# Kernel optimization log

Measured on AMD Instinct MI355X. Metric: run time of the kernel, lower is better.

The kernel has to match this reference:

```python
import jax, jax.numpy as jnp
import numpy as np

B, M, N, D = 2, 2048, 2048, 2048
N_H, D_H, D_R = 16, 128, 64
THETA = 1000000.0
SCALE = 1.0 / np.sqrt(D_H + D_R)


def build_rope_cache(seq_len, dim, theta):
    freqs = 1.0 / theta ** (jnp.arange(0, dim, 2, dtype=jnp.float32) / dim)
    t = jnp.arange(seq_len, dtype=jnp.float32)
    freqs = jnp.outer(t, freqs)  # (S, dim//2)
    cos = jnp.repeat(jnp.cos(freqs), 2, axis=-1)  # (S, dim)
    sin = jnp.repeat(jnp.sin(freqs), 2, axis=-1)
    return cos, sin


def apply_rope(x, cos, sin):
    # x: (..., S, dim); cos/sin broadcastable (S, dim)
    x_rot = jnp.stack([-x[..., 1::2], x[..., ::2]], axis=-1).reshape(x.shape)
    return x * cos + x_rot * sin


def setup_inputs() -> dict:
    key = jax.random.key(0)
    ks = jax.random.split(key, 8)
    std = 0.02
    return {
        "query": jax.random.normal(ks[0], (B, M, D), jnp.float32),
        "key_value": jax.random.normal(ks[1], (B, N, D), jnp.float32),
        "W_QC": jax.random.normal(ks[2], (N_H * D_H, D), jnp.float32) * std,
        "W_KC": jax.random.normal(ks[3], (N_H * D_H, D), jnp.float32) * std,
        "W_QR": jax.random.normal(ks[4], (N_H * D_R, D), jnp.float32) * std,
        "W_KR": jax.random.normal(ks[5], (N_H * D_R, D), jnp.float32) * std,
        "W_V": jax.random.normal(ks[6], (N_H * D_H, D), jnp.float32) * std,
        "W_O": jax.random.normal(ks[7], (D, N_H * D_H), jnp.float32) * std,
    }


def reference(query, key_value, W_QC, W_KC, W_QR, W_KR, W_V, W_O):
    # projections: torch Linear is x @ W.T
    Q_C = (query @ W_QC.T).reshape(B, M, N_H, D_H).transpose(0, 2, 1, 3)  # (B,H,M,dh)
    K_C = (key_value @ W_KC.T).reshape(B, N, N_H, D_H).transpose(0, 2, 1, 3)
    Q_R = (query @ W_QR.T).reshape(B, M, N_H, D_R).transpose(0, 2, 1, 3)  # (B,H,M,dR)
    K_R = (key_value @ W_KR.T).reshape(B, N, N_H, D_R).transpose(0, 2, 1, 3)
    cos, sin = build_rope_cache(max(M, N), D_R, THETA)
    Q_R = apply_rope(Q_R, cos[:M], sin[:M])
    K_R = apply_rope(K_R, cos[:N], sin[:N])
    scores = (jnp.einsum('bhmd,bhnd->bhmn', Q_C, K_C)
              + jnp.einsum('bhmr,bhnr->bhmn', Q_R, K_R)) * SCALE
    attn = jax.nn.softmax(scores, axis=-1)
    V = (key_value @ W_V.T).reshape(B, N, N_H, D_H).transpose(0, 2, 1, 3)
    out = jnp.einsum('bhmn,bhnd->bhmd', attn, V)  # (B,H,M,dh)
    out = out.transpose(0, 2, 1, 3).reshape(B, M, N_H * D_H)
    return out @ W_O.T
```

## Files before the change

kernel.cpp:

```cpp
#include <hip/hip_runtime.h>
#include <hip/hip_bf16.h>

typedef unsigned short u16;
typedef unsigned int u32;
typedef unsigned long long u64;
typedef __attribute__((ext_vector_type(8))) short short8;
typedef __attribute__((ext_vector_type(4))) float floatx4;

#if __has_builtin(__builtin_amdgcn_exp2f)
#define EXP2F(x) __builtin_amdgcn_exp2f(x)
#else
#define EXP2F(x) exp2f(x)
#endif

#define QSCALE (0.07216878364870323f * 1.4426950408889634f)
#define ROPE_C 0.62286151779f

__device__ __forceinline__ u16 f2b(float f) {
    unsigned int x = __builtin_bit_cast(unsigned int, f);
    unsigned int r = (x + 0x7fffu + ((x >> 16) & 1u)) >> 16;
    return (u16)r;
}
__device__ __forceinline__ u32 pk2(float a, float b) {
    return (u32)f2b(a) | ((u32)f2b(b) << 16);
}
__device__ __forceinline__ void async16(const void* g, void* l) {
    __builtin_amdgcn_global_load_lds(
        (const __attribute__((address_space(1))) void*)g,
        (__attribute__((address_space(3))) void*)l, 16, 0, 0);
}

struct CastArgs {
    const float* src[8];
    u16* dst[8];
    float scale[8];
    int startblk[8];
};

__global__ void cast_all_k(CastArgs a)
{
    const int bid = blockIdx.x;
    int s = 0;
#pragma unroll
    for (int i = 1; i < 8; ++i) s += (bid >= a.startblk[i]);
    const long idx = ((long)(bid - a.startblk[s]) * 256 + threadIdx.x) * 4;
    const float4 v = *(const float4*)(a.src[s] + idx);
    const float sc = a.scale[s];
    const u64 pk = (u64)pk2(v.x * sc, v.y * sc)
                 | ((u64)pk2(v.z * sc, v.w * sc) << 32);
    *(u64*)(a.dst[s] + idx) = pk;
}

template<int EPI>
__global__ void __launch_bounds__(256, 3)
gemm_bt(const u16* __restrict__ A, const u16* __restrict__ Bw,
        void* __restrict__ out0, u16* __restrict__ out1, u16* __restrict__ out2,
        int K)
{
    __shared__ u16 As[128 * 64];
    __shared__ u16 Bs[128 * 64];
    const int t = threadIdx.x;
    const int w = t >> 6;
    const int lane = t & 63;
    const int lq = lane >> 4, lr = lane & 15;
    const long tileM = (long)blockIdx.x * 128;
    const long tileN = (long)blockIdx.y * 128;
    const int wm = (w >> 1) * 64, wn = (w & 1) * 64;

    const floatx4 fzero = {0.f, 0.f, 0.f, 0.f};
    floatx4 acc[4][4];
#pragma unroll
    for (int i = 0; i < 4; ++i)
#pragma unroll
        for (int j = 0; j < 4; ++j) acc[i][j] = fzero;

    for (int k0 = 0; k0 < K; k0 += 64) {
#pragma unroll
        for (int r = 0; r < 4; ++r) {
            const int c = r * 256 + t;
            const int row = c >> 3, cc = c & 7;
            const int gcol = ((cc ^ (row & 7)) << 3);
            async16(A + (tileM + row) * (long)K + k0 + gcol, (char*)As + c * 16);
        }
#pragma unroll
        for (int r = 0; r < 4; ++r) {
            const int c = r * 256 + t;
            const int row = c >> 3, cc = c & 7;
            const int gcol = ((cc ^ (row & 7)) << 3);
            async16(Bw + (tileN + row) * (long)K + k0 + gcol, (char*)Bs + c * 16);
        }
        __builtin_amdgcn_s_waitcnt(0);
        __syncthreads();
#pragma unroll
        for (int kk = 0; kk < 2; ++kk) {
            short8 af[4], bfr[4];
#pragma unroll
            for (int i = 0; i < 4; ++i) {
                const int row = wm + 16 * i + lr;
                const int cc = (kk * 4 + lq) ^ (row & 7);
                af[i] = *(const short8*)(As + row * 64 + cc * 8);
            }
#pragma unroll
            for (int j = 0; j < 4; ++j) {
                const int row = wn + 16 * j + lr;
                const int cc = (kk * 4 + lq) ^ (row & 7);
                bfr[j] = *(const short8*)(Bs + row * 64 + cc * 8);
            }
#pragma unroll
            for (int i = 0; i < 4; ++i)
#pragma unroll
                for (int j = 0; j < 4; ++j)
                    acc[i][j] = __builtin_amdgcn_mfma_f32_16x16x32_bf16(
                        af[i], bfr[j], acc[i][j], 0, 0, 0);
        }
        __syncthreads();
    }

    const bool isV    = (EPI == 1) && (tileN >= 3072);
    const bool isRope = (EPI != 2) && !isV && (tileN >= 2048);

#pragma unroll
    for (int i = 0; i < 4; ++i) {
#pragma unroll
        for (int j = 0; j < 4; ++j) {
            const long row0 = tileM + wm + 16 * i + 4 * lq;
            const long col  = tileN + wn + 16 * j + lr;
            if (EPI == 2) {
#pragma unroll
                for (int r = 0; r < 4; ++r)
                    ((float*)out0)[(row0 + r) * 2048 + col] = acc[i][j][r];
            } else if (isV) {
                const u32 lo = pk2(acc[i][j][0], acc[i][j][1]);
                const u32 hi = pk2(acc[i][j][2], acc[i][j][3]);
                const long bb = row0 >> 11;
                u16* dst = out2 + ((bb * 2048 + (col - 3072)) << 11) + (row0 & 2047);
                *(uint2*)dst = make_uint2(lo, hi);
            } else if (isRope) {
                const int jj = ((int)col & 63) >> 1;
                const float freq = EXP2F(-ROPE_C * (float)jj);
#pragma unroll
                for (int r = 0; r < 4; ++r) {
                    const float v = acc[i][j][r];
                    const float vp = __shfl_xor(v, 1, 64);
                    const long row = row0 + r;
                    float sn, cs;
                    __sincosf((float)(row & 2047) * freq, &sn, &cs);
                    const float o = (col & 1) ? (v * cs + vp * sn) : (v * cs - vp * sn);
                    out1[row * 1024 + (col - 2048)] = f2b(o);
                }
            } else {
#pragma unroll
                for (int r = 0; r < 4; ++r)
                    ((u16*)out0)[(row0 + r) * 2048 + col] = f2b(acc[i][j][r]);
            }
        }
    }
}

__global__ void __launch_bounds__(256, 2)
flash_attn(const u16* __restrict__ QC, const u16* __restrict__ QR,
           const u16* __restrict__ KC, const u16* __restrict__ KR,
           const u16* __restrict__ VT, u16* __restrict__ Obuf)
{
    __shared__ u16 KC_s[64 * 128];
    __shared__ u16 KR_s[64 * 64];
    __shared__ u16 VT_s[128 * 64];
    __shared__ u16 P_s[4][32 * 72];

    const int t = threadIdx.x;
    const int w = t >> 6;
    const int lane = t & 63;
    const int lq = lane >> 4, lr = lane & 15;
    const int mbase = blockIdx.x * 128 + w * 32;
    const int h = blockIdx.y, b = blockIdx.z;

    short8 aq[2][6];
#pragma unroll
    for (int i = 0; i < 2; ++i) {
        const long m = mbase + 16 * i + lr;
        const u16* qc = QC + ((long)b * 2048 + m) * 2048 + h * 128;
        const u16* qr = QR + ((long)b * 2048 + m) * 1024 + h * 64;
#pragma unroll
        for (int kc = 0; kc < 4; ++kc) aq[i][kc]     = *(const short8*)(qc + kc * 32 + lq * 8);
#pragma unroll
        for (int kc = 0; kc < 2; ++kc) aq[i][4 + kc] = *(const short8*)(qr + kc * 32 + lq * 8);
    }

    const floatx4 fzero = {0.f, 0.f, 0.f, 0.f};
    float mst[2][4], lst[2][4];
    floatx4 oacc[2][8];
#pragma unroll
    for (int i = 0; i < 2; ++i) {
#pragma unroll
        for (int r = 0; r < 4; ++r) { mst[i][r] = -1e30f; lst[i][r] = 0.f; }
#pragma unroll
        for (int jn = 0; jn < 8; ++jn) oacc[i][jn] = fzero;
    }

    const u16* kc_g = KC + ((long)b * 2048) * 2048 + h * 128;
    const u16* kr_g = KR + ((long)b * 2048) * 1024 + h * 64;
    const u16* vt_g = VT + ((long)(b * 16 + h) * 128) * 2048;

    for (int kt = 0; kt < 32; ++kt) {
#pragma unroll
        for (int r = 0; r < 4; ++r) {
            const int c = r * 256 + t;
            const int krow = c >> 4, cc = c & 15;
            const int gc = cc ^ (krow & 7);
            async16(kc_g + (long)(kt * 64 + krow) * 2048 + gc * 8, (char*)KC_s + c * 16);
        }
#pragma unroll
        for (int r = 0; r < 2; ++r) {
            const int c = r * 256 + t;
            const int krow = c >> 3, cc = c & 7;
            const int gc = cc ^ (krow & 7);
            async16(kr_g + (long)(kt * 64 + krow) * 1024 + gc * 8, (char*)KR_s + c * 16);
        }
#pragma unroll
        for (int r = 0; r < 4; ++r) {
            const int c = r * 256 + t;
            const int drow = c >> 3, cc = c & 7;
            const int gc = cc ^ (drow & 7);
            async16(vt_g + (long)drow * 2048 + kt * 64 + gc * 8, (char*)VT_s + c * 16);
        }
        __builtin_amdgcn_s_waitcnt(0);
        __syncthreads();

        floatx4 s[2][4];
#pragma unroll
        for (int i = 0; i < 2; ++i)
#pragma unroll
            for (int j = 0; j < 4; ++j) s[i][j] = fzero;
#pragma unroll
        for (int kc = 0; kc < 6; ++kc) {
            short8 bfr[4];
#pragma unroll
            for (int j = 0; j < 4; ++j) {
                const int krow = 16 * j + lr;
                if (kc < 4) {
                    const int cc = (4 * kc + lq) ^ (krow & 7);
                    bfr[j] = *(const short8*)(KC_s + krow * 128 + cc * 8);
                } else {
                    const int cc = (4 * (kc - 4) + lq) ^ (krow & 7);
                    bfr[j] = *(const short8*)(KR_s + krow * 64 + cc * 8);
                }
            }
#pragma unroll
            for (int i = 0; i < 2; ++i)
#pragma unroll
                for (int j = 0; j < 4; ++j)
                    s[i][j] = __builtin_amdgcn_mfma_f32_16x16x32_bf16(
                        aq[i][kc], bfr[j], s[i][j], 0, 0, 0);
        }

        float rmax[2][4];
#pragma unroll
        for (int i = 0; i < 2; ++i)
#pragma unroll
            for (int r = 0; r < 4; ++r)
                rmax[i][r] = fmaxf(fmaxf(s[i][0][r], s[i][1][r]),
                                   fmaxf(s[i][2][r], s[i][3][r]));
#pragma unroll
        for (int d = 1; d < 16; d <<= 1)
#pragma unroll
            for (int i = 0; i < 2; ++i)
#pragma unroll
                for (int r = 0; r < 4; ++r)
                    rmax[i][r] = fmaxf(rmax[i][r], __shfl_xor(rmax[i][r], d, 64));

        int upd = 0;
#pragma unroll
        for (int i = 0; i < 2; ++i)
#pragma unroll
            for (int r = 0; r < 4; ++r) upd |= (rmax[i][r] > mst[i][r]);

        if (__any(upd)) {
#pragma unroll
            for (int i = 0; i < 2; ++i) {
                float alpha[4];
#pragma unroll
                for (int r = 0; r < 4; ++r) {
                    const float mnew = fmaxf(mst[i][r], rmax[i][r]);
                    alpha[r] = EXP2F(mst[i][r] - mnew);
                    mst[i][r] = mnew;
                    lst[i][r] *= alpha[r];
                }
#pragma unroll
                for (int jn = 0; jn < 8; ++jn)
#pragma unroll
                    for (int r = 0; r < 4; ++r) oacc[i][jn][r] *= alpha[r];
            }
        }

        float rsum[2][4];
#pragma unroll
        for (int i = 0; i < 2; ++i)
#pragma unroll
            for (int r = 0; r < 4; ++r) rsum[i][r] = 0.f;
#pragma unroll
        for (int i = 0; i < 2; ++i)
#pragma unroll
            for (int j = 0; j < 4; ++j)
#pragma unroll
                for (int r = 0; r < 4; ++r) {
                    const float p = EXP2F(s[i][j][r] - mst[i][r]);
                    s[i][j][r] = p;
                    rsum[i][r] += p;
                }
#pragma unroll
        for (int d = 1; d < 16; d <<= 1)
#pragma unroll
            for (int i = 0; i < 2; ++i)
#pragma unroll
                for (int r = 0; r < 4; ++r)
                    rsum[i][r] += __shfl_xor(rsum[i][r], d, 64);
#pragma unroll
        for (int i = 0; i < 2; ++i)
#pragma unroll
            for (int r = 0; r < 4; ++r) lst[i][r] += rsum[i][r];

        u16* pw = &P_s[w][0];
#pragma unroll
        for (int i = 0; i < 2; ++i)
#pragma unroll
            for (int j = 0; j < 4; ++j) {
                const u32 d0 = pk2(s[i][j][0], s[i][j][1]);
                const u32 d1 = pk2(s[i][j][2], s[i][j][3]);
                const int base = (16 * i + 4 * lq) * 72 + 16 * j + lr;
                pw[base]       = (u16)d0;
                pw[base + 72]  = (u16)(d0 >> 16);
                pw[base + 144] = (u16)d1;
                pw[base + 216] = (u16)(d1 >> 16);
            }

#pragma unroll
        for (int kc = 0; kc < 2; ++kc) {
            short8 ap[2];
#pragma unroll
            for (int i = 0; i < 2; ++i)
                ap[i] = *(const short8*)(&P_s[w][0] + (16 * i + lr) * 72 + kc * 32 + lq * 8);
#pragma unroll
            for (int jn = 0; jn < 8; ++jn) {
                const int drow = 16 * jn + lr;
                const int cc = (4 * kc + lq) ^ (drow & 7);
                const short8 bv = *(const short8*)(VT_s + drow * 64 + cc * 8);
#pragma unroll
                for (int i = 0; i < 2; ++i)
                    oacc[i][jn] = __builtin_amdgcn_mfma_f32_16x16x32_bf16(
                        ap[i], bv, oacc[i][jn], 0, 0, 0);
            }
        }
        __syncthreads();
    }

#pragma unroll
    for (int i = 0; i < 2; ++i)
#pragma unroll
        for (int jn = 0; jn < 8; ++jn)
#pragma unroll
            for (int r = 0; r < 4; ++r) {
                const long row = mbase + 16 * i + 4 * lq + r;
                const int d = 16 * jn + lr;
                const float v = oacc[i][jn][r] / lst[i][r];
                Obuf[((long)b * 2048 + row) * 2048 + h * 128 + d] = f2b(v);
            }
}

extern "C" void kernel_launch(void* const* d_in, const int* in_sizes, int n_in,
                              void* d_out, int out_size, void* d_ws, size_t ws_size,
                              hipStream_t stream)
{
    (void)in_sizes; (void)n_in; (void)out_size; (void)ws_size;

    u16* p = (u16*)d_ws;
    u16* qbf   = p; p += 8388608;
    u16* kvbf  = p; p += 8388608;
    u16* wqall = p; p += 6291456;
    u16* wkvall= p; p += 10485760;
    u16* wob   = p; p += 4194304;
    u16* QCb   = p; p += 8388608;
    u16* QRb   = p; p += 4194304;
    u16* KCb   = p; p += 8388608;
    u16* KRb   = p; p += 4194304;
    u16* VTb   = p; p += 8388608;
    u16* Ob    = p; p += 8388608;

    CastArgs a;
    a.src[0] = (const float*)d_in[0]; a.dst[0] = qbf;               a.scale[0] = QSCALE;
    a.src[1] = (const float*)d_in[1]; a.dst[1] = kvbf;              a.scale[1] = 1.f;
    a.src[2] = (const float*)d_in[2]; a.dst[2] = wqall;             a.scale[2] = 1.f;
    a.src[3] = (const float*)d_in[3]; a.dst[3] = wkvall;            a.scale[3] = 1.f;
    a.src[4] = (const float*)d_in[4]; a.dst[4] = wqall + 4194304;   a.scale[4] = 1.f;
    a.src[5] = (const float*)d_in[5]; a.dst[5] = wkvall + 4194304;  a.scale[5] = 1.f;
    a.src[6] = (const float*)d_in[6]; a.dst[6] = wkvall + 6291456;  a.scale[6] = 1.f;
    a.src[7] = (const float*)d_in[7]; a.dst[7] = wob;               a.scale[7] = 1.f;
    const int blks[8] = {8192, 8192, 4096, 4096, 2048, 2048, 4096, 4096};
    int acc = 0;
    for (int i = 0; i < 8; ++i) { a.startblk[i] = acc; acc += blks[i]; }

    cast_all_k<<<acc, 256, 0, stream>>>(a);

    gemm_bt<0><<<dim3(32, 24), 256, 0, stream>>>(qbf,  wqall,  QCb, QRb, nullptr, 2048);
    gemm_bt<1><<<dim3(32, 40), 256, 0, stream>>>(kvbf, wkvall, KCb, KRb, VTb,     2048);

    flash_attn<<<dim3(16, 16, 2), 256, 0, stream>>>(QCb, QRb, KCb, KRb, VTb, Ob);

    gemm_bt<2><<<dim3(32, 16), 256, 0, stream>>>(Ob, wob, d_out, nullptr, nullptr, 2048);
}
```

Before: 513.9 us.

## Compute transposed score tiles so each lane owns one query row

Swaps the MFMA operand order (K as A, Q as B) so the score accumulator is transposed and each lane holds a single query row's values across its four registers. Row max and row sum then need only two cross-lane shuffles instead of four per value, and the per-row softmax state shrinks from eight to two scalars per lane. The P tile and the output are written as packed 8-byte stores instead of scattered 2-byte stores, and the final normalization uses a reciprocal multiply. The P·V MFMA is also swapped to match the transposed layout, so correctness depends on the new index mapping being consistent.

```diff
diff --git a/kernel.cpp b/kernel.cpp
--- a/kernel.cpp
+++ b/kernel.cpp
@@ -187,12 +187,11 @@
     }
 
     const floatx4 fzero = {0.f, 0.f, 0.f, 0.f};
-    float mst[2][4], lst[2][4];
+    float mst[2], lst[2];
     floatx4 oacc[2][8];
 #pragma unroll
     for (int i = 0; i < 2; ++i) {
-#pragma unroll
-        for (int r = 0; r < 4; ++r) { mst[i][r] = -1e30f; lst[i][r] = 0.f; }
+        mst[i] = -1e30f; lst[i] = 0.f;
 #pragma unroll
         for (int jn = 0; jn < 8; ++jn) oacc[i][jn] = fzero;
     }
@@ -226,111 +225,89 @@
         __builtin_amdgcn_s_waitcnt(0);
         __syncthreads();
 
-        floatx4 s[2][4];
-#pragma unroll
-        for (int i = 0; i < 2; ++i)
-#pragma unroll
-            for (int j = 0; j < 4; ++j) s[i][j] = fzero;
+        floatx4 sT[4][2];
+#pragma unroll
+        for (int j = 0; j < 4; ++j)
+#pragma unroll
+            for (int i = 0; i < 2; ++i) sT[j][i] = fzero;
 #pragma unroll
         for (int kc = 0; kc < 6; ++kc) {
-            short8 bfr[4];
+            short8 kf[4];
 #pragma unroll
             for (int j = 0; j < 4; ++j) {
                 const int krow = 16 * j + lr;
                 if (kc < 4) {
                     const int cc = (4 * kc + lq) ^ (krow & 7);
-                    bfr[j] = *(const short8*)(KC_s + krow * 128 + cc * 8);
+                    kf[j] = *(const short8*)(KC_s + krow * 128 + cc * 8);
                 } else {
                     const int cc = (4 * (kc - 4) + lq) ^ (krow & 7);
-                    bfr[j] = *(const short8*)(KR_s + krow * 64 + cc * 8);
+                    kf[j] = *(const short8*)(KR_s + krow * 64 + cc * 8);
                 }
             }
 #pragma unroll
+            for (int j = 0; j < 4; ++j)
+#pragma unroll
+                for (int i = 0; i < 2; ++i)
+                    sT[j][i] = __builtin_amdgcn_mfma_f32_16x16x32_bf16(
+                        kf[j], aq[i][kc], sT[j][i], 0, 0, 0);
+        }
+
+        float rmax[2];
+#pragma unroll
+        for (int i = 0; i < 2; ++i) {
+            float a0 = fmaxf(fmaxf(sT[0][i][0], sT[0][i][1]), fmaxf(sT[0][i][2], sT[0][i][3]));
+            float a1 = fmaxf(fmaxf(sT[1][i][0], sT[1][i][1]), fmaxf(sT[1][i][2], sT[1][i][3]));
+            float a2 = fmaxf(fmaxf(sT[2][i][0], sT[2][i][1]), fmaxf(sT[2][i][2], sT[2][i][3]));
+            float a3 = fmaxf(fmaxf(sT[3][i][0], sT[3][i][1]), fmaxf(sT[3][i][2], sT[3][i][3]));
+            rmax[i] = fmaxf(fmaxf(a0, a1), fmaxf(a2, a3));
+        }
+#pragma unroll
+        for (int i = 0; i < 2; ++i) {
+            rmax[i] = fmaxf(rmax[i], __shfl_xor(rmax[i], 16, 64));
+            rmax[i] = fmaxf(rmax[i], __shfl_xor(rmax[i], 32, 64));
+        }
+
+        const int upd = (rmax[0] > mst[0]) | (rmax[1] > mst[1]);
+        if (__any(upd)) {
+#pragma unroll
+            for (int i = 0; i < 2; ++i) {
+                const float mnew = fmaxf(mst[i], rmax[i]);
+                const float alpha = EXP2F(mst[i] - mnew);
+                mst[i] = mnew;
+                lst[i] *= alpha;
+#pragma unroll
+                for (int jn = 0; jn < 8; ++jn)
+#pragma unroll
+                    for (int r = 0; r < 4; ++r) oacc[i][jn][r] *= alpha;
+            }
+        }
+
+        float rsum[2] = {0.f, 0.f};
+#pragma unroll
+        for (int j = 0; j < 4; ++j)
+#pragma unroll
             for (int i = 0; i < 2; ++i)
 #pragma unroll
-                for (int j = 0; j < 4; ++j)
-                    s[i][j] = __builtin_amdgcn_mfma_f32_16x16x32_bf16(
-                        aq[i][kc], bfr[j], s[i][j], 0, 0, 0);
-        }
-
-        float rmax[2][4];
+                for (int r = 0; r < 4; ++r) {
+                    const float p = EXP2F(sT[j][i][r] - mst[i]);
+                    sT[j][i][r] = p;
+                    rsum[i] += p;
+                }
+#pragma unroll
+        for (int i = 0; i < 2; ++i) {
+            rsum[i] += __shfl_xor(rsum[i], 16, 64);
+            rsum[i] += __shfl_xor(rsum[i], 32, 64);
+            lst[i] += rsum[i];
+        }
+
+        u16* pw = &P_s[w][0];
 #pragma unroll
         for (int i = 0; i < 2; ++i)
 #pragma unroll
-            for (int r = 0; r < 4; ++r)
-                rmax[i][r] = fmaxf(fmaxf(s[i][0][r], s[i][1][r]),
-                                   fmaxf(s[i][2][r], s[i][3][r]));
-#pragma unroll
-        for (int d = 1; d < 16; d <<= 1)
-#pragma unroll
-            for (int i = 0; i < 2; ++i)
-#pragma unroll
-                for (int r = 0; r < 4; ++r)
-                    rmax[i][r] = fmaxf(rmax[i][r], __shfl_xor(rmax[i][r], d, 64));
-
-        int upd = 0;
-#pragma unroll
-        for (int i = 0; i < 2; ++i)
-#pragma unroll
-            for (int r = 0; r < 4; ++r) upd |= (rmax[i][r] > mst[i][r]);
-
-        if (__any(upd)) {
-#pragma unroll
-            for (int i = 0; i < 2; ++i) {
-                float alpha[4];
-#pragma unroll
-                for (int r = 0; r < 4; ++r) {
-                    const float mnew = fmaxf(mst[i][r], rmax[i][r]);
-                    alpha[r] = EXP2F(mst[i][r] - mnew);
-                    mst[i][r] = mnew;
-                    lst[i][r] *= alpha[r];
-                }
-#pragma unroll
-                for (int jn = 0; jn < 8; ++jn)
-#pragma unroll
-                    for (int r = 0; r < 4; ++r) oacc[i][jn][r] *= alpha[r];
-            }
-        }
-
-        float rsum[2][4];
-#pragma unroll
-        for (int i = 0; i < 2; ++i)
-#pragma unroll
-            for (int r = 0; r < 4; ++r) rsum[i][r] = 0.f;
-#pragma unroll
-        for (int i = 0; i < 2; ++i)
-#pragma unroll
-            for (int j = 0; j < 4; ++j)
-#pragma unroll
-                for (int r = 0; r < 4; ++r) {
-                    const float p = EXP2F(s[i][j][r] - mst[i][r]);
-                    s[i][j][r] = p;
-                    rsum[i][r] += p;
-                }
-#pragma unroll
-        for (int d = 1; d < 16; d <<= 1)
-#pragma unroll
-            for (int i = 0; i < 2; ++i)
-#pragma unroll
-                for (int r = 0; r < 4; ++r)
-                    rsum[i][r] += __shfl_xor(rsum[i][r], d, 64);
-#pragma unroll
-        for (int i = 0; i < 2; ++i)
-#pragma unroll
-            for (int r = 0; r < 4; ++r) lst[i][r] += rsum[i][r];
-
-        u16* pw = &P_s[w][0];
-#pragma unroll
-        for (int i = 0; i < 2; ++i)
-#pragma unroll
             for (int j = 0; j < 4; ++j) {
-                const u32 d0 = pk2(s[i][j][0], s[i][j][1]);
-                const u32 d1 = pk2(s[i][j][2], s[i][j][3]);
-                const int base = (16 * i + 4 * lq) * 72 + 16 * j + lr;
-                pw[base]       = (u16)d0;
-                pw[base + 72]  = (u16)(d0 >> 16);
-                pw[base + 144] = (u16)d1;
-                pw[base + 216] = (u16)(d1 >> 16);
+                const u32 d0 = pk2(sT[j][i][0], sT[j][i][1]);
+                const u32 d1 = pk2(sT[j][i][2], sT[j][i][3]);
+                *(uint2*)(pw + (16 * i + lr) * 72 + 16 * j + 4 * lq) = make_uint2(d0, d1);
             }
 
 #pragma unroll
@@ -347,23 +324,24 @@
 #pragma unroll
                 for (int i = 0; i < 2; ++i)
                     oacc[i][jn] = __builtin_amdgcn_mfma_f32_16x16x32_bf16(
-                        ap[i], bv, oacc[i][jn], 0, 0, 0);
+                        bv, ap[i], oacc[i][jn], 0, 0, 0);
             }
         }
         __syncthreads();
     }
 
 #pragma unroll
-    for (int i = 0; i < 2; ++i)
-#pragma unroll
-        for (int jn = 0; jn < 8; ++jn)
-#pragma unroll
-            for (int r = 0; r < 4; ++r) {
-                const long row = mbase + 16 * i + 4 * lq + r;
-                const int d = 16 * jn + lr;
-                const float v = oacc[i][jn][r] / lst[i][r];
-                Obuf[((long)b * 2048 + row) * 2048 + h * 128 + d] = f2b(v);
-            }
+    for (int i = 0; i < 2; ++i) {
+        const float rl = 1.0f / lst[i];
+        const long row = (long)b * 2048 + mbase + 16 * i + lr;
+#pragma unroll
+        for (int jn = 0; jn < 8; ++jn) {
+            const u32 lo = pk2(oacc[i][jn][0] * rl, oacc[i][jn][1] * rl);
+            const u32 hi = pk2(oacc[i][jn][2] * rl, oacc[i][jn][3] * rl);
+            u16* dst = Obuf + row * 2048 + h * 128 + 16 * jn + 4 * lq;
+            *(uint2*)dst = make_uint2(lo, hi);
+        }
+    }
 }
 
 extern "C" void kernel_launch(void* const* d_in, const int* in_sizes, int n_in,
```

Measured after the change: 472.3 us. 8.1% less time.
